# Kernel optimization log

Hardware: AMD Instinct MI355X
Metric: run time of the kernel (lower is better)

## Reference

```python
import jax, jax.numpy as jnp
import numpy as np


def setup_inputs() -> dict:
    key = jax.random.key(0)
    ks = jax.random.split(key, 5)
    B, S, H = 64, 1024, 1024
    scale = 1.0 / np.sqrt(H)
    return {
        "decoder_hidden": jax.random.normal(ks[0], (B, H), jnp.float32),
        "encoder_outputs": jax.random.normal(ks[1], (B, S, H), jnp.float32),
        "W1": jax.random.normal(ks[2], (H, H), jnp.float32) * scale,
        "W2": jax.random.normal(ks[3], (H, H), jnp.float32) * scale,
        "v": jax.random.normal(ks[4], (H,), jnp.float32) * scale,
    }


def reference(decoder_hidden, encoder_outputs, W1, W2, v):
    # W1 @ decoder_hidden: [B, H] computed once, broadcast over src_len
    dh_proj = jnp.einsum("bh,oh->bo", decoder_hidden, W1)          # [B, H]
    enc_proj = jnp.einsum("bsh,oh->bso", encoder_outputs, W2)      # [B, S, H]
    energy = jnp.tanh(dh_proj[:, None, :] + enc_proj)              # [B, S, H]
    scores = jnp.einsum("bsh,h->bs", energy, v)                    # [B, S]
    attention_weights = jax.nn.softmax(scores, axis=-1)            # [B, S]
    context = jnp.einsum("bs,bsh->bh", attention_weights, encoder_outputs)
    return (context, attention_weights)
```

## Files before the change

### kernel.cpp

```cpp
#include <hip/hip_runtime.h>
#include <hip/hip_bf16.h>
#include <cmath>

#define Hdim 1024
#define Bdim 64
#define Sdim 1024

typedef __attribute__((ext_vector_type(4))) float f32x4;
typedef __attribute__((ext_vector_type(8))) short s16x8;
typedef __attribute__((ext_vector_type(4))) unsigned int u32x4;

static __device__ __forceinline__ unsigned short f2bf(float f) {
  unsigned int u = __builtin_bit_cast(unsigned int, f);
  unsigned int r = (u + 0x7fffu + ((u >> 16) & 1u)) >> 16;
  return (unsigned short)r;
}

static __device__ __forceinline__ float bf2f(unsigned short u) {
  return __builtin_bit_cast(float, (unsigned int)u << 16);
}

#define TANH_C 2.885390081777927f


static __device__ __forceinline__ void stage_rows64(const float* __restrict__ src,
                                                    unsigned short* As, int tid) {
  #pragma unroll 4
  for (int i = 0; i < 32; ++i) {
    int c = tid + i * 256;
    int row = c >> 7;
    int k8 = (c & 127) << 3;
    const float4* p = reinterpret_cast<const float4*>(src + row * Hdim + k8);
    float4 a = p[0];
    float4 b = p[1];
    union { unsigned short us[8]; u32x4 v; } pk;
    pk.us[0] = f2bf(a.x); pk.us[1] = f2bf(a.y); pk.us[2] = f2bf(a.z); pk.us[3] = f2bf(a.w);
    pk.us[4] = f2bf(b.x); pk.us[5] = f2bf(b.y); pk.us[6] = f2bf(b.z); pk.us[7] = f2bf(b.w);
    int idx = row * Hdim + (k8 ^ ((row & 7) << 3));
    *reinterpret_cast<u32x4*>(&As[idx]) = pk.v;
  }
}

static __device__ __forceinline__ s16x8 lda_full(const unsigned short* As, int row, int k) {
  int idx = row * Hdim + (k ^ ((row & 7) << 3));
  return *reinterpret_cast<const s16x8*>(&As[idx]);
}

static __device__ __forceinline__ s16x8 ldb_g(const unsigned short* __restrict__ Wb,
                                              const float* __restrict__ Wf,
                                              int use_bf, int o, int k) {
  if (use_bf) {
    return *reinterpret_cast<const s16x8*>(&Wb[o * Hdim + k]);
  } else {
    const float4* p = reinterpret_cast<const float4*>(Wf + o * Hdim + k);
    float4 a = p[0];
    float4 b = p[1];
    union { unsigned short us[8]; s16x8 v; } pk;
    pk.us[0] = f2bf(a.x); pk.us[1] = f2bf(a.y); pk.us[2] = f2bf(a.z); pk.us[3] = f2bf(a.w);
    pk.us[4] = f2bf(b.x); pk.us[5] = f2bf(b.y); pk.us[6] = f2bf(b.z); pk.us[7] = f2bf(b.w);
    return pk.v;
  }
}

__global__ void cast_bf16_kernel(const float* __restrict__ src,
                                 unsigned short* __restrict__ dst) {
  int i = blockIdx.x * 256 + threadIdx.x;
  const f32x4* p = reinterpret_cast<const f32x4*>(src) + i * 2;
  f32x4 a = __builtin_nontemporal_load(p);
  f32x4 b = __builtin_nontemporal_load(p + 1);
  union { unsigned short us[8]; u32x4 v; } pk;
  pk.us[0] = f2bf(a[0]); pk.us[1] = f2bf(a[1]); pk.us[2] = f2bf(a[2]); pk.us[3] = f2bf(a[3]);
  pk.us[4] = f2bf(b[0]); pk.us[5] = f2bf(b[1]); pk.us[6] = f2bf(b[2]); pk.us[7] = f2bf(b[3]);
  *reinterpret_cast<u32x4*>(dst + i * 8) = pk.v;
}

__global__ __launch_bounds__(256, 1) void proj_kernel(
    const float* __restrict__ dh, const float* __restrict__ W1f,
    const unsigned short* __restrict__ W1b, float* __restrict__ out, int use_bf) {
  __shared__ unsigned short As[64 * Hdim];
  int tid = threadIdx.x;
  stage_rows64(dh, As, tid);
  __syncthreads();
  int w = tid >> 6, lane = tid & 63;
  int lo = lane & 15, hi = lane >> 4;
  int o = blockIdx.x * 16 + lo;
  f32x4 acc = {0.f, 0.f, 0.f, 0.f};
  for (int k0 = 0; k0 < Hdim; k0 += 32) {
    int k = k0 + hi * 8;
    s16x8 bfrag = ldb_g(W1b, W1f, use_bf, o, k);
    s16x8 afrag = lda_full(As, w * 16 + lo, k);
    acc = __builtin_amdgcn_mfma_f32_16x16x32_bf16(afrag, bfrag, acc, 0, 0, 0);
  }
  #pragma unroll
  for (int r = 0; r < 4; ++r)
    out[(w * 16 + hi * 4 + r) * Hdim + o] = acc[r];
}

#define SBM 256
#define SBN 256
#define SBK 64

__global__ __launch_bounds__(512, 2) void score_mfma_kernel(
    const unsigned short* __restrict__ encb,
    const unsigned short* __restrict__ W2b,
    const float* __restrict__ dhp, const float* __restrict__ v,
    float* __restrict__ scores) {
  __shared__ unsigned short As[2][SBM * SBK];
  __shared__ unsigned short Bs[2][SBN * SBK];
  int tid = threadIdx.x;
  int bid = blockIdx.x;
  int swz = (bid & 7) * 128 + (bid >> 3);
  int mp = swz >> 2;
  int np = swz & 3;
  int row0 = mp * SBM;
  int b = row0 >> 10;
  int w = tid >> 6, lane = tid & 63;
  int wr = w >> 2, wc = w & 3;
  int lo = lane & 15, hi = lane >> 4;
  int xorv = (lo & 7) << 4;

  int srow = tid >> 3;
  int gc = (tid & 7) ^ (srow & 7);
  const unsigned short* gA0 = encb + (size_t)(row0 + srow) * Hdim + gc * 8;
  const unsigned short* gB0 = W2b + (size_t)(np * SBN + srow) * Hdim + gc * 8;

  auto SA = [&](int g, int t, int s) {
    __builtin_amdgcn_global_load_lds(
        (const __attribute__((address_space(1))) unsigned int*)(gA0 + (size_t)g * 64 * Hdim + t * SBK),
        (__attribute__((address_space(3))) unsigned int*)(&As[s][(g * 512 + w * 64) * 8]), 16, 0, 0);
  };
  auto SB = [&](int g, int t, int s) {
    __builtin_amdgcn_global_load_lds(
        (const __attribute__((address_space(1))) unsigned int*)(gB0 + (size_t)g * 64 * Hdim + t * SBK),
        (__attribute__((address_space(3))) unsigned int*)(&Bs[s][(g * 512 + w * 64) * 8]), 16, 0, 0);
  };

  f32x4 acc[2][2][4][2] = {};
  s16x8 af[2][4][2];
  s16x8 bf[2][2];

  auto LD_AF = [&](int mh_, const char* Ab) {
    #pragma unroll
    for (int m = 0; m < 4; ++m)
      #pragma unroll
      for (int ks = 0; ks < 2; ++ks)
        af[mh_][m][ks] = *reinterpret_cast<const s16x8*>(
            Ab + (mh_ * 128 + wr * 64 + m * 16 + lo) * 128 + ((ks * 64 + hi * 16) ^ xorv));
  };
  auto LD_BF = [&](int nh_, const char* Bb) {
    #pragma unroll
    for (int n = 0; n < 2; ++n)
      #pragma unroll
      for (int ks = 0; ks < 2; ++ks)
        bf[n][ks] = *reinterpret_cast<const s16x8*>(
            Bb + (nh_ * 128 + wc * 32 + n * 16 + lo) * 128 + ((ks * 64 + hi * 16) ^ xorv));
  };

  auto MFMA16 = [&](int mh_, int nh_) {
    __builtin_amdgcn_s_setprio(1);
    #pragma unroll
    for (int ks = 0; ks < 2; ++ks)
      #pragma unroll
      for (int m = 0; m < 4; ++m)
        #pragma unroll
        for (int n = 0; n < 2; ++n)
          acc[mh_][nh_][m][n] = __builtin_amdgcn_mfma_f32_16x16x32_bf16(
              af[mh_][m][ks], bf[n][ks], acc[mh_][nh_][m][n], 0, 0, 0);
    __builtin_amdgcn_s_setprio(0);
  };

  SA(0, 0, 0); SA(1, 0, 0); SB(0, 0, 0); SB(1, 0, 0);
  SA(2, 0, 0); SA(3, 0, 0); SB(2, 0, 0); SB(3, 0, 0);
  asm volatile("s_waitcnt vmcnt(0)" ::: "memory");
  __builtin_amdgcn_s_barrier();
  asm volatile("" ::: "memory");

  for (int g = 0; g < 16; ++g) {
    int rb = g & 1;
    int sb = rb ^ 1;
    int st = (g < 15) ? g + 1 : 15;
    const char* Ab = (const char*)As[rb];
    const char* Bb = (const char*)Bs[rb];

    SA(0, st, sb); SA(1, st, sb);
    LD_AF(0, Ab);
    LD_BF(0, Bb);
    __builtin_amdgcn_s_barrier();
    asm volatile("s_waitcnt lgkmcnt(0)" ::: "memory");
    MFMA16(0, 0);
    __builtin_amdgcn_s_barrier();
    asm volatile("" ::: "memory");

    SB(0, st, sb); SB(1, st, sb);
    LD_AF(1, Ab);
    __builtin_amdgcn_s_barrier();
    asm volatile("s_waitcnt lgkmcnt(0)" ::: "memory");
    MFMA16(1, 0);
    __builtin_amdgcn_s_barrier();
    asm volatile("" ::: "memory");

    SA(2, st, sb); SA(3, st, sb);
    LD_BF(1, Bb);
    __builtin_amdgcn_s_barrier();
    asm volatile("s_waitcnt lgkmcnt(0)" ::: "memory");
    MFMA16(1, 1);
    __builtin_amdgcn_s_barrier();
    asm volatile("" ::: "memory");

    SB(2, st, sb); SB(3, st, sb);
    asm volatile("s_waitcnt vmcnt(4)" ::: "memory");
    __builtin_amdgcn_s_barrier();
    MFMA16(0, 1);
    __builtin_amdgcn_s_barrier();
    asm volatile("" ::: "memory");
  }

  float psum[2][4][4] = {};
  #pragma unroll
  for (int nh = 0; nh < 2; ++nh)
    #pragma unroll
    for (int n = 0; n < 2; ++n) {
      int o = np * SBN + nh * 128 + wc * 32 + n * 16 + lo;
      float dv = dhp[b * Hdim + o];
      float vv = v[o];
      float vv2 = 2.f * vv;
      #pragma unroll
      for (int mh = 0; mh < 2; ++mh)
        #pragma unroll
        for (int m = 0; m < 4; ++m)
          #pragma unroll
          for (int r = 0; r < 4; ++r) {
            float x = acc[mh][nh][m][n][r] + dv;
            float e2 = __builtin_amdgcn_exp2f(x * TANH_C);
            float rc = __builtin_amdgcn_rcpf(1.f + e2);
            psum[mh][m][r] += vv - vv2 * rc;
          }
    }
  #pragma unroll
  for (int mask = 1; mask < 16; mask <<= 1)
    #pragma unroll
    for (int mh = 0; mh < 2; ++mh)
      #pragma unroll
      for (int m = 0; m < 4; ++m)
        #pragma unroll
        for (int r = 0; r < 4; ++r)
          psum[mh][m][r] += __shfl_xor(psum[mh][m][r], mask, 64);
  if (lo == 0) {
    #pragma unroll
    for (int mh = 0; mh < 2; ++mh)
      #pragma unroll
      for (int m = 0; m < 4; ++m)
        #pragma unroll
        for (int r = 0; r < 4; ++r)
          atomicAdd(&scores[row0 + mh * 128 + wr * 64 + m * 16 + hi * 4 + r], psum[mh][m][r]);
  }
}

#define BKt 64

__global__ __launch_bounds__(256, 3) void score_kernel(
    const float* __restrict__ enc, const float* __restrict__ W2f,
    const unsigned short* __restrict__ W2b, const float* __restrict__ dhp,
    const float* __restrict__ v, float* __restrict__ scores, int use_bf) {
  __shared__ unsigned short As[64 * BKt];
  int tid = threadIdx.x;
  int bid = blockIdx.x;
  int f = (bid & 7) * 512 + (bid >> 3);
  int rg = f >> 2;
  int oc = f & 3;
  int row0 = rg * 64;
  int b = row0 >> 10;
  int w = tid >> 6, lane = tid & 63;
  int lo = lane & 15, hi = lane >> 4;
  int n0 = oc * 256 + w * 64;

  const unsigned short* pB[4];
  const float* pBf[4];
  #pragma unroll
  for (int n = 0; n < 4; ++n) {
    int o = n0 + n * 16 + lo;
    pB[n]  = W2b + (size_t)o * Hdim + hi * 8;
    pBf[n] = W2f + (size_t)o * Hdim + hi * 8;
  }

  f32x4 acc[4][4] = {};

  for (int t = 0; t < 16; ++t) {
    int k0 = t * BKt;
    __syncthreads();
    #pragma unroll
    for (int cc = 0; cc < 2; ++cc) {
      int c = tid + cc * 256;
      int row = c >> 3;
      int j = c & 7;
      const float4* p = reinterpret_cast<const float4*>(
          enc + (size_t)(row0 + row) * Hdim + k0 + j * 8);
      float4 a = p[0];
      float4 bb = p[1];
      union { unsigned short us[8]; u32x4 v4; } pk;
      pk.us[0] = f2bf(a.x);  pk.us[1] = f2bf(a.y);  pk.us[2] = f2bf(a.z);  pk.us[3] = f2bf(a.w);
      pk.us[4] = f2bf(bb.x); pk.us[5] = f2bf(bb.y); pk.us[6] = f2bf(bb.z); pk.us[7] = f2bf(bb.w);
      int idx = row * BKt + ((j * 8) ^ ((row & 7) << 3));
      *reinterpret_cast<u32x4*>(&As[idx]) = pk.v4;
    }
    __syncthreads();

    #pragma unroll
    for (int ks = 0; ks < 2; ++ks) {
      s16x8 bfrag[4];
      #pragma unroll
      for (int n = 0; n < 4; ++n) {
        if (use_bf) {
          bfrag[n] = *reinterpret_cast<const s16x8*>(pB[n] + ks * 32);
        } else {
          const float4* p = reinterpret_cast<const float4*>(pBf[n] + ks * 32);
          float4 a = p[0];
          float4 bb = p[1];
          union { unsigned short us[8]; s16x8 v4; } pk;
          pk.us[0] = f2bf(a.x);  pk.us[1] = f2bf(a.y);  pk.us[2] = f2bf(a.z);  pk.us[3] = f2bf(a.w);
          pk.us[4] = f2bf(bb.x); pk.us[5] = f2bf(bb.y); pk.us[6] = f2bf(bb.z); pk.us[7] = f2bf(bb.w);
          bfrag[n] = pk.v4;
        }
      }
      #pragma unroll
      for (int m = 0; m < 4; ++m) {
        int kk = ks * 32 + hi * 8;
        s16x8 afrag = *reinterpret_cast<const s16x8*>(
            &As[(m * 16 + lo) * BKt + (kk ^ ((lo & 7) << 3))]);
        #pragma unroll
        for (int n = 0; n < 4; ++n)
          acc[m][n] = __builtin_amdgcn_mfma_f32_16x16x32_bf16(afrag, bfrag[n], acc[m][n], 0, 0, 0);
      }
    }
    #pragma unroll
    for (int n = 0; n < 4; ++n) { pB[n] += BKt; pBf[n] += BKt; }
  }

  float psum[4][4] = {};
  #pragma unroll
  for (int n = 0; n < 4; ++n) {
    int o = n0 + n * 16 + lo;
    float dv = dhp[b * Hdim + o];
    float vv = v[o];
    float vv2 = 2.f * vv;
    #pragma unroll
    for (int m = 0; m < 4; ++m)
      #pragma unroll
      for (int r = 0; r < 4; ++r) {
        float x = acc[m][n][r] + dv;
        float e2 = __builtin_amdgcn_exp2f(x * TANH_C);
        float rc = __builtin_amdgcn_rcpf(1.f + e2);
        psum[m][r] += vv - vv2 * rc;
      }
  }
  #pragma unroll
  for (int mask = 1; mask < 16; mask <<= 1)
    #pragma unroll
    for (int m = 0; m < 4; ++m)
      #pragma unroll
      for (int r = 0; r < 4; ++r)
        psum[m][r] += __shfl_xor(psum[m][r], mask, 64);
  if (lo == 0) {
    #pragma unroll
    for (int m = 0; m < 4; ++m)
      #pragma unroll
      for (int r = 0; r < 4; ++r)
        atomicAdd(&scores[row0 + m * 16 + hi * 4 + r], psum[m][r]);
  }
}

__global__ __launch_bounds__(256, 1) void softmax_kernel(float* __restrict__ attn) {
  __shared__ float redm[4];
  __shared__ float reds[4];
  int b = blockIdx.x, tid = threadIdx.x;
  float4 x = *reinterpret_cast<float4*>(attn + b * Sdim + tid * 4);
  float m = fmaxf(fmaxf(x.x, x.y), fmaxf(x.z, x.w));
  #pragma unroll
  for (int mask = 1; mask < 64; mask <<= 1) m = fmaxf(m, __shfl_xor(m, mask, 64));
  if ((tid & 63) == 0) redm[tid >> 6] = m;
  __syncthreads();
  m = fmaxf(fmaxf(redm[0], redm[1]), fmaxf(redm[2], redm[3]));
  float4 e;
  e.x = expf(x.x - m); e.y = expf(x.y - m); e.z = expf(x.z - m); e.w = expf(x.w - m);
  float s = e.x + e.y + e.z + e.w;
  #pragma unroll
  for (int mask = 1; mask < 64; mask <<= 1) s += __shfl_xor(s, mask, 64);
  if ((tid & 63) == 0) reds[tid >> 6] = s;
  __syncthreads();
  s = reds[0] + reds[1] + reds[2] + reds[3];
  float inv = 1.f / s;
  e.x *= inv; e.y *= inv; e.z *= inv; e.w *= inv;
  *reinterpret_cast<float4*>(attn + b * Sdim + tid * 4) = e;
}

__global__ __launch_bounds__(256, 1) void context_bf_kernel(
    const unsigned short* __restrict__ encb, const float* __restrict__ attn,
    float* __restrict__ ctx) {
  int b = blockIdx.x >> 4;
  int chunk = blockIdx.x & 15;
  int tid = threadIdx.x;
  int h0 = tid * 4;
  const unsigned short* ebase = encb + ((size_t)(b * Sdim + chunk * 64)) * Hdim + h0;
  const float* abase = attn + b * Sdim + chunk * 64;
  float4 acc = {0.f, 0.f, 0.f, 0.f};
  #pragma unroll 4
  for (int s = 0; s < 64; ++s) {
    float wgt = abase[s];
    ushort4 ev = *reinterpret_cast<const ushort4*>(ebase + (size_t)s * Hdim);
    acc.x += wgt * bf2f(ev.x);
    acc.y += wgt * bf2f(ev.y);
    acc.z += wgt * bf2f(ev.z);
    acc.w += wgt * bf2f(ev.w);
  }
  float* c = ctx + b * Hdim + h0;
  atomicAdd(c + 0, acc.x);
  atomicAdd(c + 1, acc.y);
  atomicAdd(c + 2, acc.z);
  atomicAdd(c + 3, acc.w);
}

__global__ __launch_bounds__(256, 1) void context_kernel(
    const float* __restrict__ enc, const float* __restrict__ attn,
    float* __restrict__ ctx) {
  int b = blockIdx.x >> 3;
  int chunk = blockIdx.x & 7;
  int tid = threadIdx.x;
  int h0 = tid * 4;
  const float* ebase = enc + ((size_t)(b * Sdim + chunk * 128)) * Hdim + h0;
  const float* abase = attn + b * Sdim + chunk * 128;
  float4 acc = {0.f, 0.f, 0.f, 0.f};
  #pragma unroll 4
  for (int s = 0; s < 128; ++s) {
    float wgt = abase[s];
    float4 ev = *reinterpret_cast<const float4*>(ebase + (size_t)s * Hdim);
    acc.x += wgt * ev.x; acc.y += wgt * ev.y; acc.z += wgt * ev.z; acc.w += wgt * ev.w;
  }
  float* c = ctx + b * Hdim + h0;
  atomicAdd(c + 0, acc.x);
  atomicAdd(c + 1, acc.y);
  atomicAdd(c + 2, acc.z);
  atomicAdd(c + 3, acc.w);
}

extern "C" void kernel_launch(void* const* d_in, const int* in_sizes, int n_in,
                              void* d_out, int out_size, void* d_ws, size_t ws_size,
                              hipStream_t stream) {
  const float* dh  = (const float*)d_in[0];
  const float* enc = (const float*)d_in[1];
  const float* W1  = (const float*)d_in[2];
  const float* W2  = (const float*)d_in[3];
  const float* v   = (const float*)d_in[4];
  float* out_ctx  = (float*)d_out;
  float* out_attn = out_ctx + Bdim * Hdim;

  int use_bf = (ws_size >= 4ull * 1024 * 1024) ? 1 : 0;
  int big_ws = (ws_size >= 133ull * 1024 * 1024) ? 1 : 0;
  unsigned short* W1b  = (unsigned short*)d_ws;
  unsigned short* W2b  = W1b + 1024 * 1024;
  unsigned short* encb = W2b + 1024 * 1024;

  if (use_bf) {
    cast_bf16_kernel<<<512, 256, 0, stream>>>(W1, W1b);
    cast_bf16_kernel<<<512, 256, 0, stream>>>(W2, W2b);
  }
  if (big_ws) {
    cast_bf16_kernel<<<32768, 256, 0, stream>>>(enc, encb);
  }

  proj_kernel<<<64, 256, 0, stream>>>(dh, W1, W1b, out_ctx, use_bf);

  hipMemsetAsync(out_attn, 0, (size_t)Bdim * Sdim * sizeof(float), stream);
  if (big_ws) {
    score_mfma_kernel<<<1024, 512, 0, stream>>>(encb, W2b, out_ctx, v, out_attn);
  } else {
    score_kernel<<<4096, 256, 0, stream>>>(enc, W2, W2b, out_ctx, v, out_attn, use_bf);
  }

  softmax_kernel<<<Bdim, 256, 0, stream>>>(out_attn);

  hipMemsetAsync(out_ctx, 0, (size_t)Bdim * Hdim * sizeof(float), stream);
  if (big_ws) {
    context_bf_kernel<<<1024, 256, 0, stream>>>(encb, out_attn, out_ctx);
  } else {
    context_kernel<<<512, 256, 0, stream>>>(enc, out_attn, out_ctx);
  }
}
```

Measured before the change: 305.1 us.

## Fuse encoder fp32-to-bf16 cast into score GEMM A-tile staging

Removes the separate cast kernel for the encoder tensor. The score GEMM now loads fp32 encoder rows into registers, converts them to bf16, and writes them into swizzled LDS. Blocks with np==0 also write the bf16 copy to workspace for the later context kernel. This saves one full fp32 read and a bf16 round trip of the 256MB encoder tensor. In exchange, each of the four column blocks re-reads the fp32 A tile, register pressure rises, and the pipeline barriers and waitcnt placement are restructured.

```diff
diff --git a/kernel.cpp b/kernel.cpp
--- a/kernel.cpp
+++ b/kernel.cpp
@@ -66,8 +66,8 @@
                                  unsigned short* __restrict__ dst) {
   int i = blockIdx.x * 256 + threadIdx.x;
   const f32x4* p = reinterpret_cast<const f32x4*>(src) + i * 2;
-  f32x4 a = __builtin_nontemporal_load(p);
-  f32x4 b = __builtin_nontemporal_load(p + 1);
+  f32x4 a = p[0];
+  f32x4 b = p[1];
   union { unsigned short us[8]; u32x4 v; } pk;
   pk.us[0] = f2bf(a[0]); pk.us[1] = f2bf(a[1]); pk.us[2] = f2bf(a[2]); pk.us[3] = f2bf(a[3]);
   pk.us[4] = f2bf(b[0]); pk.us[5] = f2bf(b[1]); pk.us[6] = f2bf(b[2]); pk.us[7] = f2bf(b[3]);
@@ -101,10 +101,11 @@
 #define SBK 64
 
 __global__ __launch_bounds__(512, 2) void score_mfma_kernel(
-    const unsigned short* __restrict__ encb,
+    const float* __restrict__ enc,
     const unsigned short* __restrict__ W2b,
     const float* __restrict__ dhp, const float* __restrict__ v,
-    float* __restrict__ scores) {
+    float* __restrict__ scores,
+    unsigned short* __restrict__ encb) {
   __shared__ unsigned short As[2][SBM * SBK];
   __shared__ unsigned short Bs[2][SBN * SBK];
   int tid = threadIdx.x;
@@ -118,26 +119,50 @@
   int wr = w >> 2, wc = w & 3;
   int lo = lane & 15, hi = lane >> 4;
   int xorv = (lo & 7) << 4;
+  int wr_encb = (np == 0);
 
   int srow = tid >> 3;
-  int gc = (tid & 7) ^ (srow & 7);
-  const unsigned short* gA0 = encb + (size_t)(row0 + srow) * Hdim + gc * 8;
-  const unsigned short* gB0 = W2b + (size_t)(np * SBN + srow) * Hdim + gc * 8;
-
-  auto SA = [&](int g, int t, int s) {
-    __builtin_amdgcn_global_load_lds(
-        (const __attribute__((address_space(1))) unsigned int*)(gA0 + (size_t)g * 64 * Hdim + t * SBK),
-        (__attribute__((address_space(3))) unsigned int*)(&As[s][(g * 512 + w * 64) * 8]), 16, 0, 0);
-  };
+  int gcB = (tid & 7) ^ (srow & 7);
+  const unsigned short* gB0 = W2b + (size_t)(np * SBN + srow) * Hdim + gcB * 8;
   auto SB = [&](int g, int t, int s) {
     __builtin_amdgcn_global_load_lds(
         (const __attribute__((address_space(1))) unsigned int*)(gB0 + (size_t)g * 64 * Hdim + t * SBK),
         (__attribute__((address_space(3))) unsigned int*)(&Bs[s][(g * 512 + w * 64) * 8]), 16, 0, 0);
   };
 
+  int arow = tid >> 2;
+  int q4 = tid & 3;
+  auto A_ISSUE = [&](int half, int t, f32x4* regs) {
+    const float* src = enc + (size_t)(row0 + half * 128 + arow) * Hdim + t * SBK + q4 * 16;
+    #pragma unroll
+    for (int j = 0; j < 4; ++j)
+      regs[j] = *reinterpret_cast<const f32x4*>(src + j * 4);
+  };
+  auto A_WRITE = [&](int half, int s, int t, f32x4* regs) {
+    union { unsigned short us[16]; u32x4 q[2]; } pk;
+    #pragma unroll
+    for (int j = 0; j < 4; ++j) {
+      pk.us[j * 4 + 0] = f2bf(regs[j][0]);
+      pk.us[j * 4 + 1] = f2bf(regs[j][1]);
+      pk.us[j * 4 + 2] = f2bf(regs[j][2]);
+      pk.us[j * 4 + 3] = f2bf(regs[j][3]);
+    }
+    int lrow = half * 128 + arow;
+    unsigned short* base = &As[s][lrow * 64];
+    int c0 = q4 * 2;
+    *reinterpret_cast<u32x4*>(base + ((c0 * 8) ^ ((arow & 7) * 8))) = pk.q[0];
+    *reinterpret_cast<u32x4*>(base + (((c0 + 1) * 8) ^ ((arow & 7) * 8))) = pk.q[1];
+    if (wr_encb) {
+      unsigned short* dst = encb + (size_t)(row0 + lrow) * Hdim + t * SBK + q4 * 16;
+      __builtin_nontemporal_store(pk.q[0], reinterpret_cast<u32x4*>(dst));
+      __builtin_nontemporal_store(pk.q[1], reinterpret_cast<u32x4*>(dst + 8));
+    }
+  };
+
   f32x4 acc[2][2][4][2] = {};
   s16x8 af[2][4][2];
   s16x8 bf[2][2];
+  f32x4 ar0[4], ar1[4];
 
   auto LD_AF = [&](int mh_, const char* Ab) {
     #pragma unroll
@@ -155,7 +180,6 @@
         bf[n][ks] = *reinterpret_cast<const s16x8*>(
             Bb + (nh_ * 128 + wc * 32 + n * 16 + lo) * 128 + ((ks * 64 + hi * 16) ^ xorv));
   };
-
   auto MFMA16 = [&](int mh_, int nh_) {
     __builtin_amdgcn_s_setprio(1);
     #pragma unroll
@@ -169,9 +193,11 @@
     __builtin_amdgcn_s_setprio(0);
   };
 
-  SA(0, 0, 0); SA(1, 0, 0); SB(0, 0, 0); SB(1, 0, 0);
-  SA(2, 0, 0); SA(3, 0, 0); SB(2, 0, 0); SB(3, 0, 0);
+  SB(0, 0, 0); SB(1, 0, 0); SB(2, 0, 0); SB(3, 0, 0);
+  A_ISSUE(0, 0, ar0); A_ISSUE(1, 0, ar1);
   asm volatile("s_waitcnt vmcnt(0)" ::: "memory");
+  A_WRITE(0, 0, 0, ar0); A_WRITE(1, 0, 0, ar1);
+  asm volatile("s_waitcnt lgkmcnt(0)" ::: "memory");
   __builtin_amdgcn_s_barrier();
   asm volatile("" ::: "memory");
 
@@ -182,37 +208,35 @@
     const char* Ab = (const char*)As[rb];
     const char* Bb = (const char*)Bs[rb];
 
-    SA(0, st, sb); SA(1, st, sb);
+    SB(0, st, sb); SB(1, st, sb);
+    A_ISSUE(0, st, ar0);
     LD_AF(0, Ab);
     LD_BF(0, Bb);
     __builtin_amdgcn_s_barrier();
-    asm volatile("s_waitcnt lgkmcnt(0)" ::: "memory");
+    asm volatile("" ::: "memory");
     MFMA16(0, 0);
+
+    SB(2, st, sb); SB(3, st, sb);
+    A_ISSUE(1, st, ar1);
+    LD_AF(1, Ab);
     __builtin_amdgcn_s_barrier();
     asm volatile("" ::: "memory");
-
-    SB(0, st, sb); SB(1, st, sb);
-    LD_AF(1, Ab);
-    __builtin_amdgcn_s_barrier();
+    MFMA16(1, 0);
+
+    asm volatile("s_waitcnt vmcnt(6)" ::: "memory");
+    A_WRITE(0, sb, st, ar0);
+    LD_BF(1, Bb);
     asm volatile("s_waitcnt lgkmcnt(0)" ::: "memory");
-    MFMA16(1, 0);
     __builtin_amdgcn_s_barrier();
     asm volatile("" ::: "memory");
-
-    SA(2, st, sb); SA(3, st, sb);
-    LD_BF(1, Bb);
-    __builtin_amdgcn_s_barrier();
+    MFMA16(1, 1);
+
+    asm volatile("s_waitcnt vmcnt(2)" ::: "memory");
+    A_WRITE(1, sb, st, ar1);
     asm volatile("s_waitcnt lgkmcnt(0)" ::: "memory");
-    MFMA16(1, 1);
     __builtin_amdgcn_s_barrier();
     asm volatile("" ::: "memory");
-
-    SB(2, st, sb); SB(3, st, sb);
-    asm volatile("s_waitcnt vmcnt(4)" ::: "memory");
-    __builtin_amdgcn_s_barrier();
     MFMA16(0, 1);
-    __builtin_amdgcn_s_barrier();
-    asm volatile("" ::: "memory");
   }
 
   float psum[2][4][4] = {};
@@ -454,7 +478,7 @@
   float* out_attn = out_ctx + Bdim * Hdim;
 
   int use_bf = (ws_size >= 4ull * 1024 * 1024) ? 1 : 0;
-  int big_ws = (ws_size >= 133ull * 1024 * 1024) ? 1 : 0;
+  int big_ws = (ws_size >= 133ull * 1024 * 1024 && use_bf) ? 1 : 0;
   unsigned short* W1b  = (unsigned short*)d_ws;
   unsigned short* W2b  = W1b + 1024 * 1024;
   unsigned short* encb = W2b + 1024 * 1024;
@@ -463,15 +487,12 @@
     cast_bf16_kernel<<<512, 256, 0, stream>>>(W1, W1b);
     cast_bf16_kernel<<<512, 256, 0, stream>>>(W2, W2b);
   }
-  if (big_ws) {
-    cast_bf16_kernel<<<32768, 256, 0, stream>>>(enc, encb);
-  }
 
   proj_kernel<<<64, 256, 0, stream>>>(dh, W1, W1b, out_ctx, use_bf);
 
   hipMemsetAsync(out_attn, 0, (size_t)Bdim * Sdim * sizeof(float), stream);
   if (big_ws) {
-    score_mfma_kernel<<<1024, 512, 0, stream>>>(encb, W2b, out_ctx, v, out_attn);
+    score_mfma_kernel<<<1024, 512, 0, stream>>>(enc, W2b, out_ctx, v, out_attn, encb);
   } else {
     score_kernel<<<4096, 256, 0, stream>>>(enc, W2, W2b, out_ctx, v, out_attn, use_bf);
   }
```

New measurement: 408.9 us. 34.0% more time.
